# Kernel optimization log

Measured on AMD Instinct MI355X. Metric: run time of the kernel, lower is better.

## Reference

```python
import jax, jax.numpy as jnp
import numpy as np

EPS = 2e-05
N_H_RDG = 9   # lifting scale grid: h_j = 2**j, j=0..8
N_H_CROP = 3  # group-conv scale support: offsets 0,1,2 (dyadic index shifts)


def _scaled_kernel(w, h):
    """Resample base kernel w [O, I, K] (taps on integers centered at 0) at
    coordinates x/h via linear interpolation -> [O, I, (K-1)*h+1], with the
    R+ Haar-measure normalization 1/h (psi_h(x) = psi(x/h)/h)."""
    K = w.shape[-1]
    Kh = (K - 1) * h + 1
    m = jnp.arange(K, dtype=jnp.float32) - K // 2
    x = (jnp.arange(Kh, dtype=jnp.float32) - Kh // 2) / h
    hat = jnp.maximum(0.0, 1.0 - jnp.abs(x[:, None] - m[None, :]))  # [Kh, K]
    return jnp.einsum('oim,xm->oix', w, hat) / h


def _conv1d_same(x, k):
    pad = (k.shape[-1] - 1) // 2
    return jax.lax.conv_general_dilated(
        x, k, window_strides=(1,), padding=[(pad, pad)],
        dimension_numbers=('NCH', 'OIH', 'NCH'))


def _pool_r1(x, stride):
    # max pool over the spatial (last) axis only: kernel 4, pad 1 each side
    return jax.lax.reduce_window(
        x, -jnp.inf, jax.lax.max,
        window_dimensions=(1, 1, 1, 4), window_strides=(1, 1, 1, stride),
        padding=((0, 0), (0, 0), (0, 0), (1, 1)))


def _bn(x, g, b):
    # BatchNorm2d over [B, C, H_scale, L], training-mode batch stats
    mu = jnp.mean(x, axis=(0, 2, 3), keepdims=True)
    var = jnp.var(x, axis=(0, 2, 3), keepdims=True)
    return (x - mu) * jax.lax.rsqrt(var + EPS) * g[None, :, None, None] + b[None, :, None, None]


def _forward(x, w1, w2, w3, g1, b1, g2, b2, g3, b3, fw1, fb1, fw2, fb2, fw3, fb3):
    B = x.shape[0]
    # --- c1: GConvRdG lifting, scales h_j = 2**j, j=0..8 ---
    out = jnp.stack([_conv1d_same(x, _scaled_kernel(w1, 2 ** j))
                     for j in range(N_H_RDG)], axis=2)      # [B,16,9,16]
    out = _bn(jax.nn.relu(_pool_r1(out, 2)), g1, b1)        # [B,16,9,8]
    # --- c2: GConvGG, h_crop=True: out scale j uses in scales j..j+2 ---
    O2, I2 = w2.shape[0], w2.shape[1]
    w2r = w2.reshape(O2, I2 * N_H_CROP, 3)
    H2 = out.shape[2] - (N_H_CROP - 1)  # 7
    out = jnp.stack([
        _conv1d_same(out[:, :, j:j + N_H_CROP, :].reshape(B, I2 * N_H_CROP, -1),
                     _scaled_kernel(w2r, 2 ** j))
        for j in range(H2)], axis=2)                        # [B,32,7,8]
    out = _bn(jax.nn.relu(_pool_r1(out, 2)), g2, b2)        # [B,32,7,4]
    # --- c3: GConvGG with 1x1 spatial kernel ---
    w3s = w3[:, :, :, 0]  # [64,32,3]
    H3 = out.shape[2] - (N_H_CROP - 1)  # 5
    out = jnp.stack([
        jnp.einsum('oik,bikl->bol', w3s, out[:, :, j:j + N_H_CROP, :]) / (2.0 ** j)
        for j in range(H3)], axis=2)                        # [B,64,5,4]
    out = _bn(jax.nn.relu(_pool_r1(out, 4)), g3, b3)        # [B,64,5,1]
    # --- MLP head (dropout is identity in eval) ---
    out = out.reshape(B, -1)                                # [B,320]
    out = out @ fw1.T + fb1
    out = out @ fw2.T + fb2
    return out @ fw3.T + fb3                                # [B,17]


def setup_inputs() -> dict:
    key = jax.random.key(0)
    ks = jax.random.split(key, 7)
    B = 4096
    x = jax.random.normal(ks[0], (B, 6, 16), dtype=jnp.float32)
    w1 = jax.random.normal(ks[1], (16, 6, 7), dtype=jnp.float32) * (6 * 7) ** -0.5
    w2 = jax.random.normal(ks[2], (32, 16, 3, 3), dtype=jnp.float32) * (16 * 3 * 3) ** -0.5
    w3 = jax.random.normal(ks[3], (64, 32, 3, 1), dtype=jnp.float32) * (32 * 3) ** -0.5
    fw1 = jax.random.normal(ks[4], (16, 320), dtype=jnp.float32) * 320 ** -0.5
    fw2 = jax.random.normal(ks[5], (16, 16), dtype=jnp.float32) * 16 ** -0.5
    fw3 = jax.random.normal(ks[6], (17, 16), dtype=jnp.float32) * 16 ** -0.5
    return {
        'x': x, 'w1': w1, 'w2': w2, 'w3': w3,
        'g1': jnp.ones(16), 'b1': jnp.zeros(16),
        'g2': jnp.ones(32), 'b2': jnp.zeros(32),
        'g3': jnp.ones(64), 'b3': jnp.zeros(64),
        'fw1': fw1, 'fb1': jnp.zeros(16),
        'fw2': fw2, 'fb2': jnp.zeros(16),
        'fw3': fw3, 'fb3': jnp.zeros(17),
    }


def reference(x, w1, w2, w3, g1, b1, g2, b2, g3, b3, fw1, fb1, fw2, fb2, fw3, fb3):
    return _forward(x, w1, w2, w3, g1, b1, g2, b2, g3, b3, fw1, fb1, fw2, fb2, fw3, fb3)
```

## Files before the change

kernel.cpp:

```cpp
#include <hip/hip_runtime.h>

#define EPS 2e-5f

using short8  = __attribute__((ext_vector_type(8))) short;
using floatx4 = __attribute__((ext_vector_type(4))) float;

static __device__ inline unsigned short f2bf(float f) {
    unsigned u = __float_as_uint(f);
    u += 0x7fffu + ((u >> 16) & 1u);
    return (unsigned short)(u >> 16);
}


__global__ void __launch_bounds__(256) kS(const float* __restrict__ w1,
                                          unsigned short* __restrict__ W1f,
                                          float* __restrict__ stats) {
    int gid = blockIdx.x * 256 + threadIdx.x;
    if (gid < 256) stats[gid] = 0.f;
    if (gid >= 221184) return;
    int j  = gid / 24576;
    int r  = gid % 24576;
    int T  = r / 1536;
    int r2 = r % 1536;
    int ks = r2 / 512;
    int r3 = r2 % 512;
    int ln = r3 >> 3, e = r3 & 7;
    int n  = T * 16 + (ln & 15);
    int kk = ks * 32 + (ln >> 4) * 8 + e;
    int o = n >> 4, t = n & 15;
    int i = kk >> 4, s = kk & 15;
    int h = 1 << j;
    int d = s - t;
    float val = 0.f;
    if (d >= -3 * h && d <= 3 * h) {
        float df = (float)d / (float)h;
        #pragma unroll
        for (int m = 0; m < 7; ++m) {
            float hat = fmaxf(0.f, 1.f - fabsf(df - (float)(m - 3)));
            val += w1[(o * 6 + i) * 7 + m] * hat;
        }
        val /= (float)h;
    }
    W1f[gid] = f2bf(val);
}

__global__ void __launch_bounds__(256) k1(const float* __restrict__ x,
                                          const unsigned short* __restrict__ W1f,
                                          unsigned short* __restrict__ p1,
                                          float* __restrict__ stats1, int B) {
    __shared__ float z[32 * 276];
    __shared__ float lsS[256], lsQ[256];
    int tid = threadIdx.x, j = blockIdx.y;
    int wav = tid >> 6, lane = tid & 63;
    int quad = lane >> 4, l15 = lane & 15;
    int msub = wav & 1, nh = wav >> 1;
    int b0 = blockIdx.x * 32;
    floatx4 acc[8];
    #pragma unroll
    for (int T = 0; T < 8; ++T) acc[T] = floatx4{0.f, 0.f, 0.f, 0.f};
    const float* xr = x + (size_t)(b0 + msub * 16 + l15) * 96;
    const short8* Bj = (const short8*)W1f + (size_t)(j * 16) * 3 * 64;
    #pragma unroll
    for (int ks = 0; ks < 3; ++ks) {
        int k0 = ks * 32 + quad * 8;
        floatx4 v0 = *(const floatx4*)(xr + k0);
        floatx4 v1 = *(const floatx4*)(xr + k0 + 4);
        short8 a;
        #pragma unroll
        for (int e = 0; e < 4; ++e) {
            a[e]     = (short)f2bf(v0[e]);
            a[e + 4] = (short)f2bf(v1[e]);
        }
        #pragma unroll
        for (int T = 0; T < 8; ++T) {
            short8 b = Bj[((nh * 8 + T) * 3 + ks) * 64 + lane];
            acc[T] = __builtin_amdgcn_mfma_f32_16x16x32_bf16(a, b, acc[T], 0, 0, 0);
        }
    }
    #pragma unroll
    for (int T = 0; T < 8; ++T) {
        int col = (nh * 8 + T) * 16 + l15;
        int rb  = msub * 16 + quad * 4;
        #pragma unroll
        for (int r = 0; r < 4; ++r) z[(rb + r) * 276 + col] = acc[T][r];
    }
    __syncthreads();
    float psum = 0.f, pss = 0.f;
    #pragma unroll
    for (int i = 0; i < 2; ++i) {
        int u = tid + 256 * i;
        int row = u >> 4, o = u & 15;
        const float* zr = &z[row * 276 + o * 16];
        floatx4 q0 = ((const floatx4*)zr)[0];
        floatx4 q1 = ((const floatx4*)zr)[1];
        floatx4 q2 = ((const floatx4*)zr)[2];
        floatx4 q3 = ((const floatx4*)zr)[3];
        float t[16] = {q0[0], q0[1], q0[2], q0[3], q1[0], q1[1], q1[2], q1[3],
                       q2[0], q2[1], q2[2], q2[3], q3[0], q3[1], q3[2], q3[3]};
        short8 pk;
        #pragma unroll
        for (int tp = 0; tp < 8; ++tp) {
            int lo = (tp == 0) ? 0 : 2 * tp - 1;
            int hi = (tp == 7) ? 15 : 2 * tp + 2;
            float m = t[lo];
            for (int tt = lo + 1; tt <= hi; ++tt) m = fmaxf(m, t[tt]);
            m = fmaxf(m, 0.f);
            pk[tp] = (short)f2bf(m);
            psum += m; pss += m * m;
        }
        *(short8*)(p1 + ((size_t)j * B + b0 + row) * 128 + o * 8) = pk;
    }
    lsS[(tid & 15) * 16 + (tid >> 4)] = psum;
    lsQ[(tid & 15) * 16 + (tid >> 4)] = pss;
    __syncthreads();
    if (tid < 32) {
        int o = tid & 15;
        const float* src = (tid < 16) ? lsS : lsQ;
        float s = 0.f;
        #pragma unroll
        for (int g = 0; g < 16; ++g) s += src[o * 16 + g];
        atomicAdd(&stats1[(tid < 16 ? 0 : 16) + o], s);
    }
}

__global__ void __launch_bounds__(384) k_bias(const float* __restrict__ w2,
                                              const float* __restrict__ g1,
                                              const float* __restrict__ b1,
                                              const float* __restrict__ stats1,
                                              unsigned short* __restrict__ W2f,
                                              float* __restrict__ bias2,
                                              float invN1) {
    int blk = blockIdx.x;
    int j   = blk >> 8;
    int col = blk & 255;
    int o = col >> 3, t = col & 7;
    int k = threadIdx.x;
    int ic = k >> 3, s = k & 7;
    int i = ic / 3, c = ic % 3;
    float mu  = stats1[i] * invN1;
    float var = stats1[16 + i] * invN1 - mu * mu;
    float rsg = rsqrtf(var + EPS);
    float a1  = g1[i] * rsg;
    float d1  = b1[i] - mu * a1;
    int h = 1 << j;
    int d = s - t;
    float raw = 0.f;
    if (d >= -h && d <= h) {
        float df = (float)d / (float)h;
        #pragma unroll
        for (int m = 0; m < 3; ++m) {
            float hat = fmaxf(0.f, 1.f - fabsf(df - (float)(m - 1)));
            raw += w2[((o * 16 + i) * 3 + c) * 3 + m] * hat;
        }
        raw /= (float)h;
    }
    {
        int T    = col >> 4;
        int lane = (col & 15) + ((k >> 3) & 3) * 16;
        int ks   = k >> 5;
        int e    = k & 7;
        W2f[(((size_t)(j * 16 + T) * 12 + ks) * 64 + lane) * 8 + e] = f2bf(raw * a1);
    }
    __shared__ float red[384];
    red[k] = raw * d1;
    __syncthreads();
    if (k < 128) red[k] += red[k + 128] + red[k + 256];
    __syncthreads();
    for (int st = 64; st >= 1; st >>= 1) {
        if (k < st) red[k] += red[k + st];
        __syncthreads();
    }
    if (k == 0) bias2[j * 256 + col] = red[0];
}

__global__ void __launch_bounds__(256) k2(const unsigned short* __restrict__ p1,
                                          const unsigned short* __restrict__ W2f,
                                          const float* __restrict__ bias2,
                                          unsigned short* __restrict__ p2s,
                                          float* __restrict__ stats2, int B) {
    __shared__ float z[32 * 260];
    __shared__ unsigned short pt[4][64][40];
    __shared__ float lsS[512], lsQ[512];
    int tid = threadIdx.x, j = blockIdx.y;
    int wav = tid >> 6, lane = tid & 63;
    int quad = lane >> 4, l15 = lane & 15;
    int nh = wav & 1, mp = wav >> 1;
    int b0 = blockIdx.x * 64, m0 = b0 + mp * 32;
    floatx4 acc[2][8];
    #pragma unroll
    for (int mi = 0; mi < 2; ++mi)
        #pragma unroll
        for (int T = 0; T < 8; ++T) acc[mi][T] = floatx4{0.f, 0.f, 0.f, 0.f};
    const short8* Bj = (const short8*)W2f + (size_t)(j * 16) * 12 * 64;
    #pragma unroll
    for (int ks = 0; ks < 12; ++ks) {
        int icq = ks * 4 + quad;
        int i = icq / 3, c = icq - i * 3;
        const unsigned short* ap = p1 + ((size_t)(j + c) * B + m0 + l15) * 128 + i * 8;
        short8 a0 = *(const short8*)ap;
        short8 a1 = *(const short8*)(ap + 2048);
        #pragma unroll
        for (int T = 0; T < 8; ++T) {
            short8 b = Bj[((nh * 8 + T) * 12 + ks) * 64 + lane];
            acc[0][T] = __builtin_amdgcn_mfma_f32_16x16x32_bf16(a0, b, acc[0][T], 0, 0, 0);
            acc[1][T] = __builtin_amdgcn_mfma_f32_16x16x32_bf16(a1, b, acc[1][T], 0, 0, 0);
        }
    }
    float biasv[8];
    #pragma unroll
    for (int T = 0; T < 8; ++T) biasv[T] = bias2[j * 256 + (nh * 8 + T) * 16 + l15];
    float psum[2] = {0.f, 0.f}, pss[2] = {0.f, 0.f};
    for (int pass = 0; pass < 2; ++pass) {
        __syncthreads();
        if (mp == pass) {
            #pragma unroll
            for (int T = 0; T < 8; ++T) {
                int col = (nh * 8 + T) * 16 + l15;
                #pragma unroll
                for (int mi = 0; mi < 2; ++mi) {
                    int rb = mi * 16 + quad * 4;
                    #pragma unroll
                    for (int r = 0; r < 4; ++r)
                        z[(rb + r) * 260 + col] = acc[mi][T][r] + biasv[T];
                }
            }
        }
        __syncthreads();
        #pragma unroll
        for (int i2 = 0; i2 < 2; ++i2) {
            int u = tid + 256 * i2;
            int opr = u & 15, row = u >> 4;
            const float* zr = &z[row * 260 + opr * 16];
            floatx4 q0 = ((const floatx4*)zr)[0];
            floatx4 q1 = ((const floatx4*)zr)[1];
            floatx4 q2 = ((const floatx4*)zr)[2];
            floatx4 q3 = ((const floatx4*)zr)[3];
            float ta[8] = {q0[0], q0[1], q0[2], q0[3], q1[0], q1[1], q1[2], q1[3]};
            float tb[8] = {q2[0], q2[1], q2[2], q2[3], q3[0], q3[1], q3[2], q3[3]};
            int rowg = pass * 32 + row;
            #pragma unroll
            for (int tp = 0; tp < 4; ++tp) {
                int lo = (tp == 0) ? 0 : 2 * tp - 1;
                int hi = (tp == 3) ? 7 : 2 * tp + 2;
                float m0v = ta[lo], m1v = tb[lo];
                for (int tt = lo + 1; tt <= hi; ++tt) {
                    m0v = fmaxf(m0v, ta[tt]); m1v = fmaxf(m1v, tb[tt]);
                }
                m0v = fmaxf(m0v, 0.f); m1v = fmaxf(m1v, 0.f);
                psum[0] += m0v; pss[0] += m0v * m0v;
                psum[1] += m1v; pss[1] += m1v * m1v;
                unsigned pk = (unsigned)f2bf(m0v) | ((unsigned)f2bf(m1v) << 16);
                *(unsigned*)&pt[tp][rowg][opr * 2] = pk;
            }
        }
    }
    {
        int o0 = 2 * (tid & 15), g = tid >> 4;
        lsS[o0 * 16 + g] = psum[0]; lsS[(o0 + 1) * 16 + g] = psum[1];
        lsQ[o0 * 16 + g] = pss[0];  lsQ[(o0 + 1) * 16 + g] = pss[1];
    }
    __syncthreads();
    #pragma unroll
    for (int tp = 0; tp < 4; ++tp) {
        int oct = tid & 3, row = (tid >> 2) & 63;
        *(short8*)(p2s + ((size_t)(j * 4 + tp) * B + b0 + row) * 32 + oct * 8) =
            *(const short8*)&pt[tp][row][oct * 8];
    }
    if (tid < 64) {
        int o = tid & 31;
        const float* src = (tid < 32) ? lsS : lsQ;
        float s = 0.f;
        #pragma unroll
        for (int g = 0; g < 16; ++g) s += src[o * 16 + g];
        atomicAdd(&stats2[(tid < 32 ? 0 : 32) + o], s);
    }
}

__global__ void __launch_bounds__(256) k3(const unsigned short* __restrict__ p2s,
                                          const float* __restrict__ w3,
                                          const float* __restrict__ g2,
                                          const float* __restrict__ b2,
                                          const float* __restrict__ stats2,
                                          unsigned short* __restrict__ act3,
                                          float* __restrict__ stats3,
                                          float invN2, int B) {
    __shared__ float a2s[32], d2s[32];
    __shared__ unsigned short atile[32][72];
    __shared__ float lsS[1024], lsQ[1024];
    int tid = threadIdx.x, j = blockIdx.y, b0 = blockIdx.x * 32;
    int og = tid >> 6, lane = tid & 63;
    int quad = lane >> 4, l15 = lane & 15;
    if (tid < 32) {
        float mu  = stats2[tid] * invN2;
        float var = stats2[32 + tid] * invN2 - mu * mu;
        float rs  = rsqrtf(var + EPS);
        a2s[tid] = g2[tid] * rs;
        d2s[tid] = b2[tid] - mu * a2s[tid];
    }
    __syncthreads();
    int o = og * 16 + l15;
    float biasacc = 0.f;
    short8 af[3];
    #pragma unroll
    for (int kf = 0; kf < 3; ++kf) {
        short8 v;
        #pragma unroll
        for (int e = 0; e < 8; ++e) {
            int i = quad * 8 + e;
            float raw = w3[o * 96 + i * 3 + kf];
            v[e] = (short)f2bf(raw * a2s[i]);
            biasacc = fmaf(raw, d2s[i], biasacc);
        }
        af[kf] = v;
    }
    biasacc += __shfl_xor(biasacc, 16, 64);
    biasacc += __shfl_xor(biasacc, 32, 64);
    float brow[4];
    #pragma unroll
    for (int r = 0; r < 4; ++r) brow[r] = __shfl(biasacc, quad * 4 + r, 64);
    float inv = 1.f / (float)(1 << j);
    float psum[4] = {0.f, 0.f, 0.f, 0.f}, pss[4] = {0.f, 0.f, 0.f, 0.f};
    #pragma unroll
    for (int bt = 0; bt < 2; ++bt) {
        int bb = b0 + bt * 16;
        floatx4 aL0 = {0.f, 0.f, 0.f, 0.f};
        floatx4 aL1 = {0.f, 0.f, 0.f, 0.f};
        floatx4 aL2 = {0.f, 0.f, 0.f, 0.f};
        #pragma unroll
        for (int c = 0; c < 3; ++c) {
            const unsigned short* base =
                p2s + ((size_t)((j + c) * 4) * B + bb + l15) * 32 + quad * 8;
            short8 f0 = *(const short8*)base;
            short8 f1 = *(const short8*)(base + (size_t)B * 32);
            short8 f2v = *(const short8*)(base + (size_t)2 * B * 32);
            aL0 = __builtin_amdgcn_mfma_f32_16x16x32_bf16(af[c], f0, aL0, 0, 0, 0);
            aL1 = __builtin_amdgcn_mfma_f32_16x16x32_bf16(af[c], f1, aL1, 0, 0, 0);
            aL2 = __builtin_amdgcn_mfma_f32_16x16x32_bf16(af[c], f2v, aL2, 0, 0, 0);
        }
        #pragma unroll
        for (int r = 0; r < 4; ++r) {
            float vm = fmaxf(fmaxf(aL0[r], aL1[r]), aL2[r]);
            float v  = fmaxf((vm + brow[r]) * inv, 0.f);
            atile[bt * 16 + l15][og * 16 + quad * 4 + r] = f2bf(v);
            psum[r] += v; pss[r] += v * v;
        }
    }
    #pragma unroll
    for (int r = 0; r < 4; ++r) {
        lsS[(og * 16 + quad * 4 + r) * 16 + l15] = psum[r];
        lsQ[(og * 16 + quad * 4 + r) * 16 + l15] = pss[r];
    }
    __syncthreads();
    {
        int row = tid >> 3, oct = tid & 7;
        *(short8*)(act3 + ((size_t)j * B + b0 + row) * 64 + oct * 8) =
            *(const short8*)&atile[row][oct * 8];
    }
    if (tid < 128) {
        int oo = tid & 63;
        const float* src = (tid < 64) ? lsS : lsQ;
        float s = 0.f;
        #pragma unroll
        for (int g = 0; g < 16; ++g) s += src[oo * 16 + g];
        atomicAdd(&stats3[(tid < 64 ? 0 : 64) + oo], s);
    }
}

__global__ void __launch_bounds__(64) k4(const unsigned short* __restrict__ act3,
                                         const float* __restrict__ g3,
                                         const float* __restrict__ b3,
                                         const float* __restrict__ stats3,
                                         const float* __restrict__ fw1,
                                         const float* __restrict__ fb1,
                                         const float* __restrict__ fw2,
                                         const float* __restrict__ fb2,
                                         const float* __restrict__ fw3,
                                         const float* __restrict__ fb3,
                                         float* __restrict__ out,
                                         float invN3, int B) {
    __shared__ float a3s[64], d3s[64];
    __shared__ unsigned short W1s[5120];
    __shared__ float fw2s[256], fw3s[272], fb2s[16], fb3s[17], fb1f[16], tmp[4][16];
    __shared__ float hbuf[16][17];
    int tid = threadIdx.x, lane = tid;
    int quad = lane >> 4, l15 = lane & 15;
    {
        float mu  = stats3[tid] * invN3;
        float var = stats3[64 + tid] * invN3 - mu * mu;
        float rs  = rsqrtf(var + EPS);
        a3s[tid] = g3[tid] * rs;
        d3s[tid] = b3[tid] - mu * a3s[tid];
    }
    __syncthreads();
    #pragma unroll 4
    for (int k = 0; k < 80; ++k) {
        int idx = tid + 64 * k;
        int e  = idx & 7;
        int ln = (idx >> 3) & 63;
        int fs = idx >> 9;
        int jj = fs >> 1, ks = fs & 1;
        int n = ln & 15;
        int oo = ks * 32 + (ln >> 4) * 8 + e;
        W1s[idx] = f2bf(fw1[n * 320 + oo * 5 + jj] * a3s[oo]);
    }
    #pragma unroll
    for (int k = 0; k < 4; ++k) fw2s[tid + 64 * k] = fw2[tid + 64 * k];
    for (int idx = tid; idx < 272; idx += 64) fw3s[idx] = fw3[idx];
    if (tid < 16) fb2s[tid] = fb2[tid];
    if (tid < 17) fb3s[tid] = fb3[tid];
    {
        int f = tid & 15, ch = tid >> 4;
        float s = 0.f;
        for (int u = 0; u < 80; ++u) {
            int n = ch * 80 + u;
            s = fmaf(fw1[f * 320 + n], d3s[n / 5], s);
        }
        tmp[ch][f] = s;
    }
    __syncthreads();
    if (tid < 16) fb1f[tid] = fb1[tid] + tmp[0][tid] + tmp[1][tid] + tmp[2][tid] + tmp[3][tid];
    __syncthreads();
    int mt = blockIdx.x;
    floatx4 acc = {0.f, 0.f, 0.f, 0.f};
    #pragma unroll
    for (int jj = 0; jj < 5; ++jj)
        #pragma unroll
        for (int ks = 0; ks < 2; ++ks) {
            short8 a = *(const short8*)(act3 +
                ((size_t)jj * B + mt * 16 + l15) * 64 + ks * 32 + quad * 8);
            short8 b = *(const short8*)&W1s[((jj * 2 + ks) * 64 + lane) * 8];
            acc = __builtin_amdgcn_mfma_f32_16x16x32_bf16(a, b, acc, 0, 0, 0);
        }
    #pragma unroll
    for (int r = 0; r < 4; ++r) hbuf[quad * 4 + r][l15] = acc[r] + fb1f[l15];
    __syncthreads();
    if (lane < 16) {
        int row = l15;
        float hv[16];
        #pragma unroll
        for (int n = 0; n < 16; ++n) hv[n] = hbuf[row][n];
        float h2[16];
        #pragma unroll
        for (int f2 = 0; f2 < 16; ++f2) {
            float s = fb2s[f2];
            #pragma unroll
            for (int n = 0; n < 16; ++n) s = fmaf(fw2s[f2 * 16 + n], hv[n], s);
            h2[f2] = s;
        }
        float* orow = out + (size_t)(mt * 16 + row) * 17;
        #pragma unroll
        for (int f3 = 0; f3 < 17; ++f3) {
            float s = fb3s[f3];
            #pragma unroll
            for (int n = 0; n < 16; ++n) s = fmaf(fw3s[f3 * 16 + n], h2[n], s);
            orow[f3] = s;
        }
    }
}

extern "C" void kernel_launch(void* const* d_in, const int* in_sizes, int n_in,
                              void* d_out, int out_size, void* d_ws, size_t ws_size,
                              hipStream_t stream) {
    (void)n_in; (void)out_size; (void)ws_size;
    const float* x   = (const float*)d_in[0];
    const float* w1  = (const float*)d_in[1];
    const float* w2  = (const float*)d_in[2];
    const float* w3  = (const float*)d_in[3];
    const float* g1  = (const float*)d_in[4];
    const float* b1  = (const float*)d_in[5];
    const float* g2  = (const float*)d_in[6];
    const float* b2  = (const float*)d_in[7];
    const float* g3  = (const float*)d_in[8];
    const float* b3  = (const float*)d_in[9];
    const float* fw1 = (const float*)d_in[10];
    const float* fb1 = (const float*)d_in[11];
    const float* fw2 = (const float*)d_in[12];
    const float* fb2 = (const float*)d_in[13];
    const float* fw3 = (const float*)d_in[14];
    const float* fb3 = (const float*)d_in[15];
    float* out = (float*)d_out;

    int B = in_sizes[0] / 96;

    char* wsb = (char*)d_ws;
    float*          stats = (float*)wsb;
    unsigned short* W1f   = (unsigned short*)(wsb + 1024);
    unsigned short* W2f   = W1f + 221184;
    float*          bias2 = (float*)(W2f + 688128);
    unsigned short* p1    = (unsigned short*)(bias2 + 1792);
    unsigned short* p2s   = p1 + (size_t)9 * B * 128;
    unsigned short* act3  = p2s + (size_t)28 * B * 32;

    float* stats1 = stats;
    float* stats2 = stats + 32;
    float* stats3 = stats + 96;

    float invN1 = 1.f / (float)(B * 72);
    float invN2 = 1.f / (float)(B * 28);
    float invN3 = 1.f / (float)(B * 5);

    kS<<<864, 256, 0, stream>>>(w1, W1f, stats);
    k1<<<dim3(B / 32, 9), 256, 0, stream>>>(x, W1f, p1, stats1, B);
    k_bias<<<7 * 256, 384, 0, stream>>>(w2, g1, b1, stats1, W2f, bias2, invN1);
    k2<<<dim3(B / 64, 7), 256, 0, stream>>>(p1, W2f, bias2, p2s, stats2, B);
    k3<<<dim3(B / 32, 5), 256, 0, stream>>>(p2s, w3, g2, b2, stats2, act3, stats3,
                                            invN2, B);
    k4<<<B / 16, 64, 0, stream>>>(act3, g3, b3, stats3, fw1, fb1, fw2, fb2, fw3, fb3,
                                  out, invN3, B);
}
```

Baseline: 178.2 us.

## Fold BN1 into k2, precompute stats-independent W2 and bias sums in kS

Removes the k_bias launch. kS now also builds the resampled W2 in bf16 with no BN scaling, plus per-channel kernel sums S, since neither depends on batch statistics. k2 computes the BN1 scale and shift from stats1, builds bias2 from S in shared memory, and rescales each A fragment by the per-channel scale before the MFMA. This adds bf16 round-trip rescaling work inside k2's inner loop and slightly changes rounding. In addition, k3 stages w3 in LDS, and k4 runs two waves per block with fw1 cached in LDS to amortise the per-block weight preparation.

```diff
diff --git a/kernel.cpp b/kernel.cpp
--- a/kernel.cpp
+++ b/kernel.cpp
@@ -10,38 +10,104 @@
     u += 0x7fffu + ((u >> 16) & 1u);
     return (unsigned short)(u >> 16);
 }
+static __device__ inline float bf2f(short s) {
+    return __uint_as_float(((unsigned)(unsigned short)s) << 16);
+}
+static __device__ inline short8 scale8(short8 v, float sc) {
+    short8 r;
+    #pragma unroll
+    for (int e = 0; e < 8; ++e) r[e] = (short)f2bf(bf2f(v[e]) * sc);
+    return r;
+}
 
 
 __global__ void __launch_bounds__(256) kS(const float* __restrict__ w1,
+                                          const float* __restrict__ w2,
                                           unsigned short* __restrict__ W1f,
+                                          unsigned short* __restrict__ W2r,
+                                          float* __restrict__ S,
                                           float* __restrict__ stats) {
     int gid = blockIdx.x * 256 + threadIdx.x;
     if (gid < 256) stats[gid] = 0.f;
-    if (gid >= 221184) return;
-    int j  = gid / 24576;
-    int r  = gid % 24576;
-    int T  = r / 1536;
-    int r2 = r % 1536;
-    int ks = r2 / 512;
-    int r3 = r2 % 512;
-    int ln = r3 >> 3, e = r3 & 7;
-    int n  = T * 16 + (ln & 15);
-    int kk = ks * 32 + (ln >> 4) * 8 + e;
-    int o = n >> 4, t = n & 15;
-    int i = kk >> 4, s = kk & 15;
-    int h = 1 << j;
-    int d = s - t;
-    float val = 0.f;
-    if (d >= -3 * h && d <= 3 * h) {
-        float df = (float)d / (float)h;
-        #pragma unroll
-        for (int m = 0; m < 7; ++m) {
-            float hat = fmaxf(0.f, 1.f - fabsf(df - (float)(m - 3)));
-            val += w1[(o * 6 + i) * 7 + m] * hat;
-        }
-        val /= (float)h;
-    }
-    W1f[gid] = f2bf(val);
+    if (gid < 221184) {
+        int j  = gid / 24576;
+        int r  = gid % 24576;
+        int T  = r / 1536;
+        int r2 = r % 1536;
+        int ks = r2 / 512;
+        int r3 = r2 % 512;
+        int ln = r3 >> 3, e = r3 & 7;
+        int n  = T * 16 + (ln & 15);
+        int kk = ks * 32 + (ln >> 4) * 8 + e;
+        int o = n >> 4, t = n & 15;
+        int i = kk >> 4, s = kk & 15;
+        int h = 1 << j;
+        int d = s - t;
+        float val = 0.f;
+        if (d >= -3 * h && d <= 3 * h) {
+            float df = (float)d / (float)h;
+            #pragma unroll
+            for (int m = 0; m < 7; ++m) {
+                float hat = fmaxf(0.f, 1.f - fabsf(df - (float)(m - 3)));
+                val += w1[(o * 6 + i) * 7 + m] * hat;
+            }
+            val /= (float)h;
+        }
+        W1f[gid] = f2bf(val);
+    } else if (gid < 909312) {
+        int g  = gid - 221184;
+        int fs = g >> 9;
+        int ln = (g >> 3) & 63, e = g & 7;
+        int j  = fs / 192;
+        int rm = fs % 192;
+        int T  = rm / 12, ks = rm % 12;
+        int col = T * 16 + (ln & 15);
+        int k   = ks * 32 + (ln >> 4) * 8 + e;
+        int o = col >> 3, t = col & 7;
+        int ic = k >> 3, s = k & 7;
+        int i = ic / 3, c = ic % 3;
+        int h = 1 << j;
+        int d = s - t;
+        float raw = 0.f;
+        if (d >= -h && d <= h) {
+            float df = (float)d / (float)h;
+            #pragma unroll
+            for (int m = 0; m < 3; ++m) {
+                float hat = fmaxf(0.f, 1.f - fabsf(df - (float)(m - 1)));
+                raw += w2[((o * 16 + i) * 3 + c) * 3 + m] * hat;
+            }
+            raw /= (float)h;
+        }
+        W2r[g] = f2bf(raw);
+    } else if (gid < 937984) {
+        int g = gid - 909312;
+        int j = g >> 12;
+        int r = g & 4095;
+        int i = r >> 8;
+        int col = r & 255;
+        int o = col >> 3, t = col & 7;
+        int h = 1 << j;
+        float acc = 0.f;
+        #pragma unroll
+        for (int c = 0; c < 3; ++c) {
+            const float* wr = &w2[((o * 16 + i) * 3 + c) * 3];
+            #pragma unroll
+            for (int s = 0; s < 8; ++s) {
+                int d = s - t;
+                if (d >= -h && d <= h) {
+                    float df = (float)d / (float)h;
+                    float raw = 0.f;
+                    #pragma unroll
+                    for (int m = 0; m < 3; ++m) {
+                        float hat = fmaxf(0.f, 1.f - fabsf(df - (float)(m - 1)));
+                        raw += wr[m] * hat;
+                    }
+                    acc += raw / (float)h;
+                }
+            }
+        }
+        S[g] = acc;
+    }
 }
 
 __global__ void __launch_bounds__(256) k1(const float* __restrict__ x,
@@ -123,82 +189,57 @@
     }
 }
 
-__global__ void __launch_bounds__(384) k_bias(const float* __restrict__ w2,
-                                              const float* __restrict__ g1,
-                                              const float* __restrict__ b1,
-                                              const float* __restrict__ stats1,
-                                              unsigned short* __restrict__ W2f,
-                                              float* __restrict__ bias2,
-                                              float invN1) {
-    int blk = blockIdx.x;
-    int j   = blk >> 8;
-    int col = blk & 255;
-    int o = col >> 3, t = col & 7;
-    int k = threadIdx.x;
-    int ic = k >> 3, s = k & 7;
-    int i = ic / 3, c = ic % 3;
-    float mu  = stats1[i] * invN1;
-    float var = stats1[16 + i] * invN1 - mu * mu;
-    float rsg = rsqrtf(var + EPS);
-    float a1  = g1[i] * rsg;
-    float d1  = b1[i] - mu * a1;
-    int h = 1 << j;
-    int d = s - t;
-    float raw = 0.f;
-    if (d >= -h && d <= h) {
-        float df = (float)d / (float)h;
-        #pragma unroll
-        for (int m = 0; m < 3; ++m) {
-            float hat = fmaxf(0.f, 1.f - fabsf(df - (float)(m - 1)));
-            raw += w2[((o * 16 + i) * 3 + c) * 3 + m] * hat;
-        }
-        raw /= (float)h;
-    }
-    {
-        int T    = col >> 4;
-        int lane = (col & 15) + ((k >> 3) & 3) * 16;
-        int ks   = k >> 5;
-        int e    = k & 7;
-        W2f[(((size_t)(j * 16 + T) * 12 + ks) * 64 + lane) * 8 + e] = f2bf(raw * a1);
-    }
-    __shared__ float red[384];
-    red[k] = raw * d1;
-    __syncthreads();
-    if (k < 128) red[k] += red[k + 128] + red[k + 256];
-    __syncthreads();
-    for (int st = 64; st >= 1; st >>= 1) {
-        if (k < st) red[k] += red[k + st];
-        __syncthreads();
-    }
-    if (k == 0) bias2[j * 256 + col] = red[0];
-}
-
 __global__ void __launch_bounds__(256) k2(const unsigned short* __restrict__ p1,
-                                          const unsigned short* __restrict__ W2f,
-                                          const float* __restrict__ bias2,
+                                          const unsigned short* __restrict__ W2r,
+                                          const float* __restrict__ S,
+                                          const float* __restrict__ g1,
+                                          const float* __restrict__ b1,
+                                          const float* __restrict__ stats1,
                                           unsigned short* __restrict__ p2s,
-                                          float* __restrict__ stats2, int B) {
+                                          float* __restrict__ stats2,
+                                          float invN1, int B) {
     __shared__ float z[32 * 260];
     __shared__ unsigned short pt[4][64][40];
     __shared__ float lsS[512], lsQ[512];
+    __shared__ float a1s[16], d1s[16], bias2L[256];
     int tid = threadIdx.x, j = blockIdx.y;
     int wav = tid >> 6, lane = tid & 63;
     int quad = lane >> 4, l15 = lane & 15;
     int nh = wav & 1, mp = wav >> 1;
     int b0 = blockIdx.x * 64, m0 = b0 + mp * 32;
+    if (tid < 16) {
+        float mu  = stats1[tid] * invN1;
+        float var = stats1[16 + tid] * invN1 - mu * mu;
+        float rs  = rsqrtf(var + EPS);
+        a1s[tid] = g1[tid] * rs;
+        d1s[tid] = b1[tid] - mu * a1s[tid];
+    }
+    __syncthreads();
+    {
+        float s = 0.f;
+        const float* Sj = S + (size_t)j * 4096;
+        #pragma unroll
+        for (int i = 0; i < 16; ++i) s = fmaf(d1s[i], Sj[i * 256 + tid], s);
+        bias2L[tid] = s;
+    }
+    __syncthreads();
+    float biasv[8];
+    #pragma unroll
+    for (int T = 0; T < 8; ++T) biasv[T] = bias2L[(nh * 8 + T) * 16 + l15];
     floatx4 acc[2][8];
     #pragma unroll
     for (int mi = 0; mi < 2; ++mi)
         #pragma unroll
         for (int T = 0; T < 8; ++T) acc[mi][T] = floatx4{0.f, 0.f, 0.f, 0.f};
-    const short8* Bj = (const short8*)W2f + (size_t)(j * 16) * 12 * 64;
+    const short8* Bj = (const short8*)W2r + (size_t)(j * 16) * 12 * 64;
     #pragma unroll
     for (int ks = 0; ks < 12; ++ks) {
         int icq = ks * 4 + quad;
         int i = icq / 3, c = icq - i * 3;
+        float a1v = a1s[i];
         const unsigned short* ap = p1 + ((size_t)(j + c) * B + m0 + l15) * 128 + i * 8;
-        short8 a0 = *(const short8*)ap;
-        short8 a1 = *(const short8*)(ap + 2048);
+        short8 a0 = scale8(*(const short8*)ap, a1v);
+        short8 a1 = scale8(*(const short8*)(ap + 2048), a1v);
         #pragma unroll
         for (int T = 0; T < 8; ++T) {
             short8 b = Bj[((nh * 8 + T) * 12 + ks) * 64 + lane];
@@ -206,9 +247,6 @@
             acc[1][T] = __builtin_amdgcn_mfma_f32_16x16x32_bf16(a1, b, acc[1][T], 0, 0, 0);
         }
     }
-    float biasv[8];
-    #pragma unroll
-    for (int T = 0; T < 8; ++T) biasv[T] = bias2[j * 256 + (nh * 8 + T) * 16 + l15];
     float psum[2] = {0.f, 0.f}, pss[2] = {0.f, 0.f};
     for (int pass = 0; pass < 2; ++pass) {
         __syncthreads();
@@ -284,12 +322,18 @@
                                           unsigned short* __restrict__ act3,
                                           float* __restrict__ stats3,
                                           float invN2, int B) {
+    __shared__ float w3s[6144];
     __shared__ float a2s[32], d2s[32];
     __shared__ unsigned short atile[32][72];
     __shared__ float lsS[1024], lsQ[1024];
     int tid = threadIdx.x, j = blockIdx.y, b0 = blockIdx.x * 32;
     int og = tid >> 6, lane = tid & 63;
     int quad = lane >> 4, l15 = lane & 15;
+    #pragma unroll
+    for (int u = 0; u < 6; ++u) {
+        int idx = tid * 4 + u * 1024;
+        *(floatx4*)&w3s[idx] = *(const floatx4*)&w3[idx];
+    }
     if (tid < 32) {
         float mu  = stats2[tid] * invN2;
         float var = stats2[32 + tid] * invN2 - mu * mu;
@@ -307,7 +351,7 @@
         #pragma unroll
         for (int e = 0; e < 8; ++e) {
             int i = quad * 8 + e;
-            float raw = w3[o * 96 + i * 3 + kf];
+            float raw = w3s[o * 96 + i * 3 + kf];
             v[e] = (short)f2bf(raw * a2s[i]);
             biasacc = fmaf(raw, d2s[i], biasacc);
         }
@@ -366,61 +410,68 @@
     }
 }
 
-__global__ void __launch_bounds__(64) k4(const unsigned short* __restrict__ act3,
-                                         const float* __restrict__ g3,
-                                         const float* __restrict__ b3,
-                                         const float* __restrict__ stats3,
-                                         const float* __restrict__ fw1,
-                                         const float* __restrict__ fb1,
-                                         const float* __restrict__ fw2,
-                                         const float* __restrict__ fb2,
-                                         const float* __restrict__ fw3,
-                                         const float* __restrict__ fb3,
-                                         float* __restrict__ out,
-                                         float invN3, int B) {
+__global__ void __launch_bounds__(128) k4(const unsigned short* __restrict__ act3,
+                                          const float* __restrict__ g3,
+                                          const float* __restrict__ b3,
+                                          const float* __restrict__ stats3,
+                                          const float* __restrict__ fw1,
+                                          const float* __restrict__ fb1,
+                                          const float* __restrict__ fw2,
+                                          const float* __restrict__ fb2,
+                                          const float* __restrict__ fw3,
+                                          const float* __restrict__ fb3,
+                                          float* __restrict__ out,
+                                          float invN3, int B) {
+    __shared__ float fw1L[5120];
     __shared__ float a3s[64], d3s[64];
     __shared__ unsigned short W1s[5120];
     __shared__ float fw2s[256], fw3s[272], fb2s[16], fb3s[17], fb1f[16], tmp[4][16];
-    __shared__ float hbuf[16][17];
-    int tid = threadIdx.x, lane = tid;
+    __shared__ float hbuf[2][16][17];
+    int tid = threadIdx.x;
+    int wav = tid >> 6, lane = tid & 63;
     int quad = lane >> 4, l15 = lane & 15;
-    {
+    #pragma unroll
+    for (int u = 0; u < 10; ++u) {
+        int idx = (tid + u * 128) * 4;
+        *(floatx4*)&fw1L[idx] = *(const floatx4*)&fw1[idx];
+    }
+    if (tid < 64) {
         float mu  = stats3[tid] * invN3;
         float var = stats3[64 + tid] * invN3 - mu * mu;
         float rs  = rsqrtf(var + EPS);
         a3s[tid] = g3[tid] * rs;
         d3s[tid] = b3[tid] - mu * a3s[tid];
     }
-    __syncthreads();
-    #pragma unroll 4
-    for (int k = 0; k < 80; ++k) {
-        int idx = tid + 64 * k;
+    if (tid < 16) fb2s[tid] = fb2[tid];
+    if (tid < 17) fb3s[tid] = fb3[tid];
+    #pragma unroll
+    for (int u = 0; u < 2; ++u) fw2s[tid + u * 128] = fw2[tid + u * 128];
+    for (int idx = tid; idx < 272; idx += 128) fw3s[idx] = fw3[idx];
+    __syncthreads();
+    #pragma unroll
+    for (int u = 0; u < 40; ++u) {
+        int idx = tid + u * 128;
         int e  = idx & 7;
         int ln = (idx >> 3) & 63;
         int fs = idx >> 9;
         int jj = fs >> 1, ks = fs & 1;
         int n = ln & 15;
         int oo = ks * 32 + (ln >> 4) * 8 + e;
-        W1s[idx] = f2bf(fw1[n * 320 + oo * 5 + jj] * a3s[oo]);
-    }
-    #pragma unroll
-    for (int k = 0; k < 4; ++k) fw2s[tid + 64 * k] = fw2[tid + 64 * k];
-    for (int idx = tid; idx < 272; idx += 64) fw3s[idx] = fw3[idx];
-    if (tid < 16) fb2s[tid] = fb2[tid];
-    if (tid < 17) fb3s[tid] = fb3[tid];
-    {
+        W1s[idx] = f2bf(fw1L[n * 320 + oo * 5 + jj] * a3s[oo]);
+    }
+    if (tid < 64) {
         int f = tid & 15, ch = tid >> 4;
         float s = 0.f;
         for (int u = 0; u < 80; ++u) {
             int n = ch * 80 + u;
-            s = fmaf(fw1[f * 320 + n], d3s[n / 5], s);
+            s = fmaf(fw1L[f * 320 + n], d3s[n / 5], s);
         }
         tmp[ch][f] = s;
     }
     __syncthreads();
     if (tid < 16) fb1f[tid] = fb1[tid] + tmp[0][tid] + tmp[1][tid] + tmp[2][tid] + tmp[3][tid];
     __syncthreads();
-    int mt = blockIdx.x;
+    int mt = blockIdx.x * 2 + wav;
     floatx4 acc = {0.f, 0.f, 0.f, 0.f};
     #pragma unroll
     for (int jj = 0; jj < 5; ++jj)
@@ -432,13 +483,13 @@
             acc = __builtin_amdgcn_mfma_f32_16x16x32_bf16(a, b, acc, 0, 0, 0);
         }
     #pragma unroll
-    for (int r = 0; r < 4; ++r) hbuf[quad * 4 + r][l15] = acc[r] + fb1f[l15];
+    for (int r = 0; r < 4; ++r) hbuf[wav][quad * 4 + r][l15] = acc[r] + fb1f[l15];
     __syncthreads();
     if (lane < 16) {
         int row = l15;
         float hv[16];
         #pragma unroll
-        for (int n = 0; n < 16; ++n) hv[n] = hbuf[row][n];
+        for (int n = 0; n < 16; ++n) hv[n] = hbuf[wav][row][n];
         float h2[16];
         #pragma unroll
         for (int f2 = 0; f2 < 16; ++f2) {
@@ -485,9 +536,9 @@
     char* wsb = (char*)d_ws;
     float*          stats = (float*)wsb;
     unsigned short* W1f   = (unsigned short*)(wsb + 1024);
-    unsigned short* W2f   = W1f + 221184;
-    float*          bias2 = (float*)(W2f + 688128);
-    unsigned short* p1    = (unsigned short*)(bias2 + 1792);
+    unsigned short* W2r   = W1f + 221184;
+    float*          S     = (float*)(W2r + 688128);
+    unsigned short* p1    = (unsigned short*)(S + 28672);
     unsigned short* p2s   = p1 + (size_t)9 * B * 128;
     unsigned short* act3  = p2s + (size_t)28 * B * 32;
 
@@ -499,12 +550,12 @@
     float invN2 = 1.f / (float)(B * 28);
     float invN3 = 1.f / (float)(B * 5);
 
-    kS<<<864, 256, 0, stream>>>(w1, W1f, stats);
+    kS<<<3665, 256, 0, stream>>>(w1, w2, W1f, W2r, S, stats);
     k1<<<dim3(B / 32, 9), 256, 0, stream>>>(x, W1f, p1, stats1, B);
-    k_bias<<<7 * 256, 384, 0, stream>>>(w2, g1, b1, stats1, W2f, bias2, invN1);
-    k2<<<dim3(B / 64, 7), 256, 0, stream>>>(p1, W2f, bias2, p2s, stats2, B);
+    k2<<<dim3(B / 64, 7), 256, 0, stream>>>(p1, W2r, S, g1, b1, stats1, p2s, stats2,
+                                            invN1, B);
     k3<<<dim3(B / 32, 5), 256, 0, stream>>>(p2s, w3, g2, b2, stats2, act3, stats3,
                                             invN2, B);
-    k4<<<B / 16, 64, 0, stream>>>(act3, g3, b3, stats3, fw1, fb1, fw2, fb2, fw3, fb3,
-                                  out, invN3, B);
-}
+    k4<<<B / 32, 128, 0, stream>>>(act3, g3, b3, stats3, fw1, fb1, fw2, fb2, fw3, fb3,
+                                   out, invN3, B);
+}
```

New measurement: 175.5 us. Within noise of the previous version (-1.5%).
